# Performance work log

Hardware: AMD Instinct MI355X
Metric: run time of the kernel (lower is better)

The kernel has to match this reference:

```python
import jax, jax.numpy as jnp
import numpy as np

N = 262144      # number of points
K = 16          # KNN neighbors -> fixed degree CSR
E = N * K
CLASS_DIM = 40


def setup_inputs() -> dict:
    key = jax.random.key(0)
    ks = jax.random.split(key, 12)
    x = jax.random.normal(ks[0], (N, 3), dtype=jnp.float32)
    indptr = (jnp.arange(N + 1, dtype=jnp.int32) * K)
    indices = jax.random.randint(ks[1], (E,), 0, N, dtype=jnp.int32)

    def xavier(k, fan_out, fan_in):
        bound = np.sqrt(6.0 / (fan_in + fan_out)).astype(np.float32)
        return jax.random.uniform(k, (fan_out, fan_in), dtype=jnp.float32,
                                  minval=-bound, maxval=bound)

    return {
        "x": x, "indptr": indptr, "indices": indices,
        "w1": xavier(ks[2], 64, 3),
        "w2": xavier(ks[3], 64, 64),
        "w3": xavier(ks[4], 64, 64),
        "w4": xavier(ks[5], 128, 64),
        "w5": xavier(ks[6], 1024, 192),
        "wf1": xavier(ks[7], 512, 1024),
        "wf2": xavier(ks[8], 256, 512),
        "wf3": xavier(ks[9], CLASS_DIM, 256),
    }


def reference(x, indptr, indices, w1, w2, w3, w4, w5, wf1, wf2, wf3):
    # mlp1, mlp2 (bias-free Linear + ReLU)
    h = jax.nn.relu(x @ w1.T)          # [N, 64]
    h = jax.nn.relu(h @ w2.T)          # [N, 64]

    # GraphMaxPooling: CSR neighbor max (segment-max over gathered rows)
    n = h.shape[0]
    e = indices.shape[0]
    deg = indptr[1:] - indptr[:-1]                                   # [N]
    seg = jnp.repeat(jnp.arange(n, dtype=jnp.int32), deg,
                     total_repeat_length=e)                          # [E]
    x_gm = jax.ops.segment_max(h[indices], seg, num_segments=n,
                               indices_are_sorted=True)              # [N, 64]

    # mlp3, mlp4
    h3 = jax.nn.relu(h @ w3.T)         # [N, 64]
    h4 = jax.nn.relu(h3 @ w4.T)        # [N, 128]

    # concat neighbor-pooled features with point features, mlp5
    hc = jnp.concatenate([x_gm, h4], axis=1)   # [N, 192]
    h5 = jax.nn.relu(hc @ w5.T)                # [N, 1024]

    # global max pool over points -> [1, 1024]
    g = jnp.max(h5, axis=0, keepdims=True)

    # classifier head (dropout in eval mode = identity)
    f = jax.nn.relu(g @ wf1.T)
    f = jax.nn.relu(f @ wf2.T)
    return f @ wf3.T                            # [1, class_dim]
```

## Files before the change

### kernel.cpp

```cpp
#include <hip/hip_runtime.h>
#include <hip/hip_bf16.h>
#include <stdint.h>

typedef unsigned short u16;
typedef __bf16 bf16x8 __attribute__((ext_vector_type(8)));
typedef float  f32x4  __attribute__((ext_vector_type(4)));
typedef u16    u16x8  __attribute__((ext_vector_type(8)));

__device__ __forceinline__ float bf2f(u16 u) {
    return __uint_as_float(((unsigned)u) << 16);
}
__device__ __forceinline__ u16 f2bf(float f) {
    unsigned u = __float_as_uint(f);
    u += 0x7fffu + ((u >> 16) & 1u);
    return (u16)(u >> 16);
}
__device__ __forceinline__ u16x8 maxu16(u16x8 a, u16x8 b) {
    u16x8 r;
    #pragma unroll
    for (int e = 0; e < 8; ++e) r[e] = a[e] > b[e] ? a[e] : b[e];
    return r;
}

#define MFMA16(a, b, c) __builtin_amdgcn_mfma_f32_16x16x32_bf16(a, b, c, 0, 0, 0)

__device__ u16   h2g_buf[262144 * 64];
__device__ u16   gm_buf [262144 * 64];
__device__ u16   w3b[64 * 64];
__device__ u16   w4b[128 * 64];
__device__ u16   w5t[64 * 6 * 64 * 8];
__device__ float g_buf[1024];
__device__ float f1_buf[512];
__device__ float f2_buf[256];

__global__ void k0_zero() { g_buf[threadIdx.x] = 0.f; }

__global__ void kcvt(const float* __restrict__ w3f, const float* __restrict__ w4f,
                     const float* __restrict__ w5f)
{
    int i = blockIdx.x * 256 + threadIdx.x;
    if (i < 4096)        w3b[i]        = f2bf(w3f[i]);
    else if (i < 12288)  w4b[i - 4096] = f2bf(w4f[i - 4096]);
    else {
        int o    = i - 12288;
        int e    = o & 7;
        int lane = (o >> 3) & 63;
        int sg   = o >> 9;
        int s    = sg % 6, c16 = sg / 6;
        int q    = lane >> 4, l15 = lane & 15;
        w5t[o] = f2bf(w5f[(c16 * 16 + l15) * 192 + s * 32 + q * 8 + e]);
    }
}

__global__ __launch_bounds__(256) void k1_mlp(
    const float* __restrict__ xf, const float* __restrict__ w1f,
    const float* __restrict__ w2f)
{
    __shared__ __align__(16) u16 sw1[64 * 4];
    __shared__ __align__(16) u16 sx [64 * 4];
    __shared__ __align__(16) u16 sw2[64 * 72];
    __shared__ __align__(16) u16 shA[64 * 72];
    __shared__ __align__(16) u16 sh2[64 * 72];

    const int tid = threadIdx.x;
    const int p0  = blockIdx.x * 64;

    for (int i = tid; i < 64 * 64; i += 256)
        sw2[(i >> 6) * 72 + (i & 63)] = f2bf(w2f[i]);
    if (tid < 192) {
        sw1[(tid / 3) * 4 + tid % 3] = f2bf(w1f[tid]);
        sx [(tid / 3) * 4 + tid % 3] = f2bf(xf[p0 * 3 + tid]);
    }
    __syncthreads();

    {
        int m = tid & 63, ng = tid >> 6;
        float x0 = bf2f(sx[m * 4]), x1 = bf2f(sx[m * 4 + 1]), x2 = bf2f(sx[m * 4 + 2]);
        #pragma unroll
        for (int j = 0; j < 16; ++j) {
            int n = ng * 16 + j;
            float s = x0 * bf2f(sw1[n * 4]) + x1 * bf2f(sw1[n * 4 + 1]) + x2 * bf2f(sw1[n * 4 + 2]);
            shA[m * 72 + n] = f2bf(fmaxf(s, 0.f));
        }
    }
    __syncthreads();

    const int lane = tid & 63, w = tid >> 6, q = lane >> 4, l15 = lane & 15;
    const int mrow = 16 * w;

    f32x4 acc2[4];
    #pragma unroll
    for (int nt = 0; nt < 4; ++nt) acc2[nt] = (f32x4){0.f, 0.f, 0.f, 0.f};
    #pragma unroll
    for (int s = 0; s < 2; ++s) {
        bf16x8 a = *(const bf16x8*)&shA[(mrow + l15) * 72 + s * 32 + q * 8];
        #pragma unroll
        for (int nt = 0; nt < 4; ++nt) {
            bf16x8 b = *(const bf16x8*)&sw2[(nt * 16 + l15) * 72 + s * 32 + q * 8];
            acc2[nt] = MFMA16(a, b, acc2[nt]);
        }
    }
    #pragma unroll
    for (int nt = 0; nt < 4; ++nt)
        #pragma unroll
        for (int r = 0; r < 4; ++r) {
            int m = mrow + q * 4 + r;
            sh2[m * 72 + nt * 16 + l15] = f2bf(fmaxf(acc2[nt][r], 0.f));
        }
    __syncthreads();

    {
        int row = tid >> 2, c = (tid & 3) * 16;
        *(u16x8*)&h2g_buf[(size_t)p0 * 64 + tid * 16]     = *(const u16x8*)&sh2[row * 72 + c];
        *(u16x8*)&h2g_buf[(size_t)p0 * 64 + tid * 16 + 8] = *(const u16x8*)&sh2[row * 72 + c + 8];
    }
}

__global__ __launch_bounds__(256) void k2_pool(const int* __restrict__ idx)
{
    const size_t gt = (size_t)blockIdx.x * 256 + threadIdx.x;
    const size_t p  = gt >> 3;
    const int    c  = (threadIdx.x & 7) * 8;

    u16x8 v[16];
    #pragma unroll
    for (int k = 0; k < 16; ++k) {
        int j = idx[p * 16 + k];
        v[k] = *(const u16x8*)&h2g_buf[(size_t)j * 64 + c];
    }
    u16x8 m = v[0];
    #pragma unroll
    for (int k = 1; k < 16; ++k) m = maxu16(m, v[k]);
    *(u16x8*)&gm_buf[p * 64 + c] = m;
}

__global__ __launch_bounds__(512) void k3_fused(int* __restrict__ gout)
{
    __shared__ __align__(16) u16 lds[36864];
    u16* p0  = lds;
    u16* p1  = lds + 8192;
    u16* p2  = lds + 16384;
    u16* sw3 = lds + 24576;
    u16* sw4 = lds + 28672;

    const int tid  = threadIdx.x;
    const int lane = tid & 63, w = tid >> 6, q = lane >> 4, l15 = lane & 15;
    const int mw   = w & 1, nw = w >> 1;
    const int cg   = blockIdx.x & 3;
    const size_t R0 = (size_t)(blockIdx.x >> 2) * 128;
    const int c16b = cg * 16 + nw * 4;

    {
        int r = tid >> 3, js = tid & 7;
        *(u16x8*)&sw3[r * 64 + ((js ^ r) & 7) * 8] = *(const u16x8*)&w3b[r * 64 + js * 8];
        #pragma unroll
        for (int c = 0; c < 2; ++c) {
            int i = c * 512 + tid, r4 = i >> 3, j4 = i & 7;
            *(u16x8*)&sw4[r4 * 64 + ((j4 ^ r4) & 7) * 8] = *(const u16x8*)&w4b[r4 * 64 + j4 * 8];
        }
        #pragma unroll
        for (int c = 0; c < 2; ++c) {
            int i = c * 512 + tid, ra = i >> 3, ja = i & 7;
            *(u16x8*)&p0[ra * 64 + ((ja ^ ra) & 7) * 8] =
                *(const u16x8*)&gm_buf[(R0 + ra) * 64 + ja * 8];
            *(u16x8*)&p1[ra * 64 + ((ja ^ ra) & 7) * 8] =
                *(const u16x8*)&h2g_buf[(R0 + ra) * 64 + ja * 8];
        }
    }
    __syncthreads();

    {
        f32x4 a3[4];
        #pragma unroll
        for (int nt = 0; nt < 4; ++nt) a3[nt] = (f32x4){0.f, 0.f, 0.f, 0.f};
        #pragma unroll
        for (int ss = 0; ss < 2; ++ss) {
            int js = ss * 4 + q, r = w * 16 + l15;
            bf16x8 a = *(const bf16x8*)&p1[r * 64 + ((js ^ r) & 7) * 8];
            #pragma unroll
            for (int nt = 0; nt < 4; ++nt) {
                int rw = nt * 16 + l15;
                bf16x8 b = *(const bf16x8*)&sw3[rw * 64 + ((js ^ rw) & 7) * 8];
                a3[nt] = MFMA16(a, b, a3[nt]);
            }
        }
        #pragma unroll
        for (int nt = 0; nt < 4; ++nt)
            #pragma unroll
            for (int r = 0; r < 4; ++r) {
                int m = w * 16 + q * 4 + r;
                int n = nt * 16 + l15;
                p2[m * 64 + (((n >> 3) ^ m) & 7) * 8 + (n & 7)] =
                    f2bf(fmaxf(a3[nt][r], 0.f));
            }
    }

    {
        f32x4 a4[8];
        #pragma unroll
        for (int nt = 0; nt < 8; ++nt) a4[nt] = (f32x4){0.f, 0.f, 0.f, 0.f};
        #pragma unroll
        for (int ss = 0; ss < 2; ++ss) {
            int js = ss * 4 + q, r = w * 16 + l15;
            bf16x8 a = *(const bf16x8*)&p2[r * 64 + ((js ^ r) & 7) * 8];
            #pragma unroll
            for (int nt = 0; nt < 8; ++nt) {
                int rw = nt * 16 + l15;
                bf16x8 b = *(const bf16x8*)&sw4[rw * 64 + ((js ^ rw) & 7) * 8];
                a4[nt] = MFMA16(a, b, a4[nt]);
            }
        }
        #pragma unroll
        for (int nt = 0; nt < 8; ++nt)
            #pragma unroll
            for (int r = 0; r < 4; ++r) {
                int m  = w * 16 + q * 4 + r;
                int n4 = nt * 16 + l15;
                int j  = (n4 >> 3) & 7;
                u16* dp = (nt < 4) ? p1 : p2;
                dp[m * 64 + ((j ^ m) & 7) * 8 + (n4 & 7)] = f2bf(fmaxf(a4[nt][r], 0.f));
            }
    }
    __syncthreads();

    {
        f32x4 acc[4][4];
        #pragma unroll
        for (int mt = 0; mt < 4; ++mt)
            #pragma unroll
            for (int nt = 0; nt < 4; ++nt) acc[mt][nt] = (f32x4){0.f, 0.f, 0.f, 0.f};
        #pragma unroll
        for (int s = 0; s < 6; ++s) {
            const u16* pa = (s < 2) ? p0 : ((s < 4) ? p1 : p2);
            int j = (s & 1) * 4 + q;
            bf16x8 b[4];
            #pragma unroll
            for (int nt = 0; nt < 4; ++nt)
                b[nt] = *(const bf16x8*)&w5t[(size_t)((c16b + nt) * 6 + s) * 512 + lane * 8];
            bf16x8 a[4];
            #pragma unroll
            for (int mt = 0; mt < 4; ++mt) {
                int r = mw * 64 + mt * 16 + l15;
                a[mt] = *(const bf16x8*)&pa[r * 64 + ((j ^ r) & 7) * 8];
            }
            #pragma unroll
            for (int mt = 0; mt < 4; ++mt)
                #pragma unroll
                for (int nt = 0; nt < 4; ++nt)
                    acc[mt][nt] = MFMA16(a[mt], b[nt], acc[mt][nt]);
        }

        #pragma unroll
        for (int nt = 0; nt < 4; ++nt) {
            float mx = 0.f;
            #pragma unroll
            for (int mt = 0; mt < 4; ++mt)
                #pragma unroll
                for (int e = 0; e < 4; ++e) mx = fmaxf(mx, acc[mt][nt][e]);
            mx = fmaxf(mx, __shfl_xor(mx, 16, 64));
            mx = fmaxf(mx, __shfl_xor(mx, 32, 64));
            if (q == 0)
                atomicMax(&gout[cg * 256 + nw * 64 + nt * 16 + l15], __float_as_int(mx));
        }
    }
}

__global__ void k4_f1(const float* __restrict__ wf1)
{
    int r = blockIdx.x, l = threadIdx.x;
    float s = 0.f;
    #pragma unroll
    for (int i = 0; i < 16; ++i) s += wf1[r * 1024 + i * 64 + l] * g_buf[i * 64 + l];
    #pragma unroll
    for (int o = 32; o; o >>= 1) s += __shfl_down(s, o, 64);
    if (!l) f1_buf[r] = fmaxf(s, 0.f);
}
__global__ void k4_f2(const float* __restrict__ wf2)
{
    int r = blockIdx.x, l = threadIdx.x;
    float s = 0.f;
    #pragma unroll
    for (int i = 0; i < 8; ++i) s += wf2[r * 512 + i * 64 + l] * f1_buf[i * 64 + l];
    #pragma unroll
    for (int o = 32; o; o >>= 1) s += __shfl_down(s, o, 64);
    if (!l) f2_buf[r] = fmaxf(s, 0.f);
}
__global__ void k4_out(const float* __restrict__ wf3, float* __restrict__ out)
{
    int r = blockIdx.x, l = threadIdx.x;
    float s = 0.f;
    #pragma unroll
    for (int i = 0; i < 4; ++i) s += wf3[r * 256 + i * 64 + l] * f2_buf[i * 64 + l];
    #pragma unroll
    for (int o = 32; o; o >>= 1) s += __shfl_down(s, o, 64);
    if (!l) out[r] = s;
}

extern "C" void kernel_launch(void* const* d_in, const int* in_sizes, int n_in,
                              void* d_out, int out_size, void* d_ws, size_t ws_size,
                              hipStream_t stream)
{
    (void)in_sizes; (void)n_in; (void)out_size; (void)d_ws; (void)ws_size;
    const float* x   = (const float*)d_in[0];
    const int*   idx = (const int*)d_in[2];
    const float* w1  = (const float*)d_in[3];
    const float* w2  = (const float*)d_in[4];
    const float* w3  = (const float*)d_in[5];
    const float* w4  = (const float*)d_in[6];
    const float* w5  = (const float*)d_in[7];
    const float* wf1 = (const float*)d_in[8];
    const float* wf2 = (const float*)d_in[9];
    const float* wf3 = (const float*)d_in[10];

    float* gptr;
    hipGetSymbolAddress((void**)&gptr, HIP_SYMBOL(g_buf));

    k0_zero <<<1, 1024, 0, stream>>>();
    kcvt    <<<816, 256, 0, stream>>>(w3, w4, w5);
    k1_mlp  <<<262144 / 64, 256, 0, stream>>>(x, w1, w2);
    k2_pool <<<262144 * 8 / 256, 256, 0, stream>>>(idx);
    k3_fused<<<8192, 512, 0, stream>>>((int*)gptr);
    k4_f1   <<<512, 64, 0, stream>>>(wf1);
    k4_f2   <<<256, 64, 0, stream>>>(wf2);
    k4_out  <<<40, 64, 0, stream>>>(wf3, (float*)d_out);
}
```

Before: 417.3 us.

## Fuse neighbor max-pool gather into fused MLP kernel and loop over column groups

Removes the separate pooling kernel and its gm_buf intermediate. Each 128-row block now gathers its 16 neighbors per point straight into LDS and max-reduces them there. Each block then loops over all four 256-column groups of mlp5 instead of launching four blocks per row tile. This cuts the grid from 8192 to 2048 blocks and avoids recomputing mlp3/mlp4 four times per row tile. The trade-off is that the random gather latency now sits inside the fused kernel, and the serialized column-group loop leaves fewer blocks to hide it.

```diff
diff --git a/kernel.cpp b/kernel.cpp
--- a/kernel.cpp
+++ b/kernel.cpp
@@ -25,7 +25,6 @@
 #define MFMA16(a, b, c) __builtin_amdgcn_mfma_f32_16x16x32_bf16(a, b, c, 0, 0, 0)
 
 __device__ u16   h2g_buf[262144 * 64];
-__device__ u16   gm_buf [262144 * 64];
 __device__ u16   w3b[64 * 64];
 __device__ u16   w4b[128 * 64];
 __device__ u16   w5t[64 * 6 * 64 * 8];
@@ -116,25 +115,8 @@
     }
 }
 
-__global__ __launch_bounds__(256) void k2_pool(const int* __restrict__ idx)
-{
-    const size_t gt = (size_t)blockIdx.x * 256 + threadIdx.x;
-    const size_t p  = gt >> 3;
-    const int    c  = (threadIdx.x & 7) * 8;
-
-    u16x8 v[16];
-    #pragma unroll
-    for (int k = 0; k < 16; ++k) {
-        int j = idx[p * 16 + k];
-        v[k] = *(const u16x8*)&h2g_buf[(size_t)j * 64 + c];
-    }
-    u16x8 m = v[0];
-    #pragma unroll
-    for (int k = 1; k < 16; ++k) m = maxu16(m, v[k]);
-    *(u16x8*)&gm_buf[p * 64 + c] = m;
-}
-
-__global__ __launch_bounds__(512) void k3_fused(int* __restrict__ gout)
+__global__ __launch_bounds__(512) void k3_fused(const int* __restrict__ idx,
+                                                int* __restrict__ gout)
 {
     __shared__ __align__(16) u16 lds[36864];
     u16* p0  = lds;
@@ -145,10 +127,23 @@
 
     const int tid  = threadIdx.x;
     const int lane = tid & 63, w = tid >> 6, q = lane >> 4, l15 = lane & 15;
-    const int mw   = w & 1, nw = w >> 1;
-    const int cg   = blockIdx.x & 3;
-    const size_t R0 = (size_t)(blockIdx.x >> 2) * 128;
-    const int c16b = cg * 16 + nw * 4;
+    const size_t R0 = (size_t)blockIdx.x * 128;
+
+    #pragma unroll
+    for (int c = 0; c < 2; ++c) {
+        int task = c * 512 + tid;
+        int r = task >> 3, jc = task & 7;
+        const int* ip = &idx[(R0 + r) * 16];
+        u16x8 v[16];
+        #pragma unroll
+        for (int k = 0; k < 16; ++k)
+            v[k] = *(const u16x8*)&h2g_buf[(size_t)ip[k] * 64 + jc * 8];
+        #pragma unroll
+        for (int o = 8; o; o >>= 1)
+            #pragma unroll
+            for (int k = 0; k < o; ++k) v[k] = maxu16(v[k], v[k + o]);
+        *(u16x8*)&p0[r * 64 + ((jc ^ r) & 7) * 8] = v[0];
+    }
 
     {
         int r = tid >> 3, js = tid & 7;
@@ -161,8 +156,6 @@
         #pragma unroll
         for (int c = 0; c < 2; ++c) {
             int i = c * 512 + tid, ra = i >> 3, ja = i & 7;
-            *(u16x8*)&p0[ra * 64 + ((ja ^ ra) & 7) * 8] =
-                *(const u16x8*)&gm_buf[(R0 + ra) * 64 + ja * 8];
             *(u16x8*)&p1[ra * 64 + ((ja ^ ra) & 7) * 8] =
                 *(const u16x8*)&h2g_buf[(R0 + ra) * 64 + ja * 8];
         }
@@ -223,44 +216,45 @@
     }
     __syncthreads();
 
-    {
-        f32x4 acc[4][4];
-        #pragma unroll
-        for (int mt = 0; mt < 4; ++mt)
-            #pragma unroll
-            for (int nt = 0; nt < 4; ++nt) acc[mt][nt] = (f32x4){0.f, 0.f, 0.f, 0.f};
+    #pragma unroll 1
+    for (int cg = 0; cg < 4; ++cg) {
+        f32x4 acc[8][2];
+        #pragma unroll
+        for (int mt = 0; mt < 8; ++mt)
+            #pragma unroll
+            for (int nt = 0; nt < 2; ++nt) acc[mt][nt] = (f32x4){0.f, 0.f, 0.f, 0.f};
         #pragma unroll
         for (int s = 0; s < 6; ++s) {
             const u16* pa = (s < 2) ? p0 : ((s < 4) ? p1 : p2);
             int j = (s & 1) * 4 + q;
-            bf16x8 b[4];
-            #pragma unroll
-            for (int nt = 0; nt < 4; ++nt)
-                b[nt] = *(const bf16x8*)&w5t[(size_t)((c16b + nt) * 6 + s) * 512 + lane * 8];
-            bf16x8 a[4];
-            #pragma unroll
-            for (int mt = 0; mt < 4; ++mt) {
-                int r = mw * 64 + mt * 16 + l15;
+            bf16x8 b[2];
+            #pragma unroll
+            for (int nt = 0; nt < 2; ++nt)
+                b[nt] = *(const bf16x8*)&w5t[(size_t)(((cg * 16 + w * 2 + nt) * 6 + s)) * 512 + lane * 8];
+            bf16x8 a[8];
+            #pragma unroll
+            for (int mt = 0; mt < 8; ++mt) {
+                int r = mt * 16 + l15;
                 a[mt] = *(const bf16x8*)&pa[r * 64 + ((j ^ r) & 7) * 8];
             }
             #pragma unroll
-            for (int mt = 0; mt < 4; ++mt)
+            for (int mt = 0; mt < 8; ++mt)
                 #pragma unroll
-                for (int nt = 0; nt < 4; ++nt)
+                for (int nt = 0; nt < 2; ++nt)
                     acc[mt][nt] = MFMA16(a[mt], b[nt], acc[mt][nt]);
         }
 
         #pragma unroll
-        for (int nt = 0; nt < 4; ++nt) {
+        for (int nt = 0; nt < 2; ++nt) {
             float mx = 0.f;
             #pragma unroll
-            for (int mt = 0; mt < 4; ++mt)
+            for (int mt = 0; mt < 8; ++mt)
                 #pragma unroll
                 for (int e = 0; e < 4; ++e) mx = fmaxf(mx, acc[mt][nt][e]);
             mx = fmaxf(mx, __shfl_xor(mx, 16, 64));
             mx = fmaxf(mx, __shfl_xor(mx, 32, 64));
             if (q == 0)
-                atomicMax(&gout[cg * 256 + nw * 64 + nt * 16 + l15], __float_as_int(mx));
+                atomicMax(&gout[cg * 256 + w * 32 + nt * 16 + l15], __float_as_int(mx));
         }
     }
 }
@@ -318,8 +312,7 @@
     k0_zero <<<1, 1024, 0, stream>>>();
     kcvt    <<<816, 256, 0, stream>>>(w3, w4, w5);
     k1_mlp  <<<262144 / 64, 256, 0, stream>>>(x, w1, w2);
-    k2_pool <<<262144 * 8 / 256, 256, 0, stream>>>(idx);
-    k3_fused<<<8192, 512, 0, stream>>>((int*)gptr);
+    k3_fused<<<2048, 512, 0, stream>>>(idx, (int*)gptr);
     k4_f1   <<<512, 64, 0, stream>>>(wf1);
     k4_f2   <<<256, 64, 0, stream>>>(wf2);
     k4_out  <<<40, 64, 0, stream>>>(wf3, (float*)d_out);
```

Result: slower. 474.3 us (+13.7%).
